# Kernel tuning notes

Measured on AMD Instinct MI355X. Metric: run time of the kernel, lower is better.

## Reference

```python
import jax, jax.numpy as jnp
import numpy as np

DEGREE_RES = 15
NUM_ROT = int(np.ceil(360 / DEGREE_RES))  # 24
PIXEL_SIZE = 0.0625
IM_METERS = 4.0
IM_SIZE = int(IM_METERS / PIXEL_SIZE)  # 64


def _create_rot_mat():
    angles = np.radians([i * DEGREE_RES for i in range(NUM_ROT)])
    c, s = np.cos(angles), np.sin(angles)
    rot = np.stack([
        np.stack([c, np.zeros_like(c), -s], axis=-1),
        np.stack([np.zeros_like(c), np.ones_like(c), np.zeros_like(c)], axis=-1),
        np.stack([s, np.zeros_like(c), c], axis=-1),
    ], axis=1)  # [NUM_ROT, 3, 3]
    return jnp.asarray(rot, dtype=jnp.float32)


def setup_inputs() -> dict:
    key = jax.random.key(0)
    xyz = jax.random.normal(key, (32, 16384, 3), dtype=jnp.float32)
    rot_mat = _create_rot_mat()
    return {"xyz": xyz, "rot_mat": rot_mat}


def reference(xyz, rot_mat):
    B, N, _ = xyz.shape
    R = rot_mat.shape[0]
    # rotate each point by each rotation: [B, R, N, 3]
    xyz_rot = jnp.einsum('rij,bnj->brni', rot_mat, xyz)
    # project x,z -> pixel indices (offset by half image extent, 2 meters)
    proj = jnp.round((xyz_rot[..., :2] + IM_METERS / 2) / PIXEL_SIZE).astype(jnp.int32)
    mask = ((proj[..., 0] >= 0) & (proj[..., 0] < IM_SIZE) &
            (proj[..., 1] >= 0) & (proj[..., 1] < IM_SIZE))
    # out-of-range points are zeroed -> they (faithfully) write at pixel (0,0)
    proj = proj * mask[..., None]
    vals = xyz_rot[..., 2] / 10.0  # non-occupancy branch: scatter z/10
    image = jnp.zeros((B, R, IM_SIZE, IM_SIZE), dtype=xyz.dtype)
    b = jnp.arange(B)[:, None, None]
    r = jnp.arange(R)[None, :, None]
    image = image.at[b, r, proj[..., 1], proj[..., 0]].set(vals)
    return image
```

## Files before the change

kernel.cpp:

```cpp
#include <hip/hip_runtime.h>
#include <stdint.h>

#define BB 32
#define NN 16384
#define RR 24
#define IMS 64
#define NPIX (IMS * IMS)
#define RPB 3
#define GROUPS (RR / RPB)
#define TOTAL_PIX (BB * RR * NPIX)

__global__ __launch_bounds__(1024) void rotproj_lds(
    const float* __restrict__ xyz, const float* __restrict__ rot,
    float* __restrict__ out) {
  __shared__ unsigned int img[RPB * NPIX];

  const int blk = blockIdx.x;
  const int b = blk >> 3;
  const int rg = blk & (GROUPS - 1);

  for (int i = threadIdx.x; i < RPB * NPIX; i += 1024) img[i] = 0u;

  const float* m = rot + rg * RPB * 9;
  float c0[RPB], c2[RPB], c6[RPB], c8[RPB];
#pragma unroll
  for (int rl = 0; rl < RPB; ++rl) {
    c0[rl] = m[rl * 9 + 0];
    c2[rl] = m[rl * 9 + 2];
    c6[rl] = m[rl * 9 + 6];
    c8[rl] = m[rl * 9 + 8];
  }

  __syncthreads();

  const float4* base4 = (const float4*)(xyz + (size_t)b * NN * 3);
  const int lane = threadIdx.x & 63;

#pragma unroll
  for (int iter = 0; iter < 2; ++iter) {
    const int n0 = iter * 8192 + threadIdx.x * 8;
    const int v = 6 * (n0 >> 3);
    const float4 f0 = base4[v + 0];
    const float4 f1 = base4[v + 1];
    const float4 f2 = base4[v + 2];
    const float4 f3 = base4[v + 3];
    const float4 f4 = base4[v + 4];
    const float4 f5 = base4[v + 5];

    const float xs[8] = {f0.x, f0.w, f1.z, f2.y, f3.x, f3.w, f4.z, f5.y};
    const float ys[8] = {f0.y, f1.x, f1.w, f2.z, f3.y, f4.x, f4.w, f5.z};
    const float zs[8] = {f0.z, f1.y, f2.x, f2.w, f3.z, f4.y, f5.x, f5.w};

    bool anyoob[RPB] = {false, false, false};
    unsigned int oobkey[RPB] = {0u, 0u, 0u};

#pragma unroll
    for (int j = 0; j < 8; ++j) {
      const float x = xs[j], y = ys[j], z = zs[j];

      const int py = (int)rintf(__fmaf_rn(y, 16.0f, 32.0f));
      const bool pyin = (unsigned)py < (unsigned)IMS;
      const unsigned int nkey = (unsigned)(n0 + j + 1) << 17;

#pragma unroll
      for (int rl = 0; rl < RPB; ++rl) {
        const float xr =
            __fadd_rn(__fmul_rn(c0[rl], x), __fmul_rn(c2[rl], z));
        const float zr =
            __fadd_rn(__fmul_rn(c6[rl], x), __fmul_rn(c8[rl], z));

        const int px = (int)rintf(__fmaf_rn(xr, 16.0f, 32.0f));
        const bool in = ((unsigned)px < (unsigned)IMS) & pyin;

        const unsigned int key = nkey | (__float_as_uint(zr) >> 15);

        if (in) {
          atomicMax(&img[rl * NPIX + py * IMS + px], key);
        } else {
          anyoob[rl] = true;
          oobkey[rl] = key;
        }
      }
    }

#pragma unroll
    for (int rl = 0; rl < RPB; ++rl) {
      const unsigned long long oob = __ballot(anyoob[rl]);
      if (anyoob[rl] && lane == 63 - __builtin_clzll(oob)) {
        atomicMax(&img[rl * NPIX], oobkey[rl]);
      }
    }
  }

  __syncthreads();

  float* oslice = out + ((size_t)b * RR + (size_t)rg * RPB) * NPIX;
#pragma unroll
  for (int t = 0; t < RPB * NPIX / 1024; ++t) {
    const int i = t * 1024 + threadIdx.x;
    const unsigned int k = img[i];
    const float zr = __uint_as_float((k & 0x1FFFFu) << 15);
    oslice[i] = k ? (zr / 10.0f) : 0.0f;
  }
}

extern "C" void kernel_launch(void* const* d_in, const int* in_sizes, int n_in,
                              void* d_out, int out_size, void* d_ws,
                              size_t ws_size, hipStream_t stream) {
  const float* xyz = (const float*)d_in[0];
  const float* rot = (const float*)d_in[1];
  float* out = (float*)d_out;

  rotproj_lds<<<BB * GROUPS, 1024, 0, stream>>>(xyz, rot, out);
}
```

Before: 70.36 us.

## Route out-of-bounds points to per-lane dump slots and process 16 contiguous points per thread

Out-of-range points now do an atomicMax into a per-lane dump slot in LDS instead of taking a divergent branch with per-iteration ballots. The dump slots are reduced with wave shuffles after the scatter pass and merged into pixel (0,0). Each thread now loads 12 contiguous float4s covering 16 points in one pass, replacing two iterations of 8 points. The final divide by 10 is replaced by a multiply by 0.1, which can differ from the reference in the last bit.

```diff
diff --git a/kernel.cpp b/kernel.cpp
--- a/kernel.cpp
+++ b/kernel.cpp
@@ -8,18 +8,19 @@
 #define NPIX (IMS * IMS)
 #define RPB 3
 #define GROUPS (RR / RPB)
-#define TOTAL_PIX (BB * RR * NPIX)
+#define DUMP_BASE (RPB * NPIX)
+#define LDS_WORDS (RPB * NPIX + RPB * 64)
 
 __global__ __launch_bounds__(1024) void rotproj_lds(
     const float* __restrict__ xyz, const float* __restrict__ rot,
     float* __restrict__ out) {
-  __shared__ unsigned int img[RPB * NPIX];
+  __shared__ unsigned int img[LDS_WORDS];
 
   const int blk = blockIdx.x;
   const int b = blk >> 3;
   const int rg = blk & (GROUPS - 1);
 
-  for (int i = threadIdx.x; i < RPB * NPIX; i += 1024) img[i] = 0u;
+  for (int i = threadIdx.x; i < LDS_WORDS; i += 1024) img[i] = 0u;
 
   const float* m = rot + rg * RPB * 9;
   float c0[RPB], c2[RPB], c6[RPB], c8[RPB];
@@ -34,73 +35,71 @@
   __syncthreads();
 
   const float4* base4 = (const float4*)(xyz + (size_t)b * NN * 3);
-  const int lane = threadIdx.x & 63;
+  const int t = threadIdx.x;
+  const int lane = t & 63;
+
+  float4 f[12];
+#pragma unroll
+  for (int i = 0; i < 12; ++i) f[i] = base4[12 * t + i];
+
+  float F[48];
+#pragma unroll
+  for (int i = 0; i < 12; ++i) {
+    F[4 * i + 0] = f[i].x;
+    F[4 * i + 1] = f[i].y;
+    F[4 * i + 2] = f[i].z;
+    F[4 * i + 3] = f[i].w;
+  }
 
 #pragma unroll
-  for (int iter = 0; iter < 2; ++iter) {
-    const int n0 = iter * 8192 + threadIdx.x * 8;
-    const int v = 6 * (n0 >> 3);
-    const float4 f0 = base4[v + 0];
-    const float4 f1 = base4[v + 1];
-    const float4 f2 = base4[v + 2];
-    const float4 f3 = base4[v + 3];
-    const float4 f4 = base4[v + 4];
-    const float4 f5 = base4[v + 5];
+  for (int k = 0; k < 16; ++k) {
+    const float x = F[3 * k + 0];
+    const float y = F[3 * k + 1];
+    const float z = F[3 * k + 2];
+    const int n = t * 16 + k;
 
-    const float xs[8] = {f0.x, f0.w, f1.z, f2.y, f3.x, f3.w, f4.z, f5.y};
-    const float ys[8] = {f0.y, f1.x, f1.w, f2.z, f3.y, f4.x, f4.w, f5.z};
-    const float zs[8] = {f0.z, f1.y, f2.x, f2.w, f3.z, f4.y, f5.x, f5.w};
-
-    bool anyoob[RPB] = {false, false, false};
-    unsigned int oobkey[RPB] = {0u, 0u, 0u};
-
-#pragma unroll
-    for (int j = 0; j < 8; ++j) {
-      const float x = xs[j], y = ys[j], z = zs[j];
-
-      const int py = (int)rintf(__fmaf_rn(y, 16.0f, 32.0f));
-      const bool pyin = (unsigned)py < (unsigned)IMS;
-      const unsigned int nkey = (unsigned)(n0 + j + 1) << 17;
-
-#pragma unroll
-      for (int rl = 0; rl < RPB; ++rl) {
-        const float xr =
-            __fadd_rn(__fmul_rn(c0[rl], x), __fmul_rn(c2[rl], z));
-        const float zr =
-            __fadd_rn(__fmul_rn(c6[rl], x), __fmul_rn(c8[rl], z));
-
-        const int px = (int)rintf(__fmaf_rn(xr, 16.0f, 32.0f));
-        const bool in = ((unsigned)px < (unsigned)IMS) & pyin;
-
-        const unsigned int key = nkey | (__float_as_uint(zr) >> 15);
-
-        if (in) {
-          atomicMax(&img[rl * NPIX + py * IMS + px], key);
-        } else {
-          anyoob[rl] = true;
-          oobkey[rl] = key;
-        }
-      }
-    }
+    const int py = (int)rintf(__fmaf_rn(y, 16.0f, 32.0f));
+    const bool pyin = (unsigned)py < (unsigned)IMS;
+    const unsigned int nkey = (unsigned)(n + 1) << 17;
 
 #pragma unroll
     for (int rl = 0; rl < RPB; ++rl) {
-      const unsigned long long oob = __ballot(anyoob[rl]);
-      if (anyoob[rl] && lane == 63 - __builtin_clzll(oob)) {
-        atomicMax(&img[rl * NPIX], oobkey[rl]);
-      }
+      const float xr = __fadd_rn(__fmul_rn(c0[rl], x), __fmul_rn(c2[rl], z));
+      const float zr = __fadd_rn(__fmul_rn(c6[rl], x), __fmul_rn(c8[rl], z));
+
+      const int px = (int)rintf(__fmaf_rn(xr, 16.0f, 32.0f));
+      const bool in = ((unsigned)px < (unsigned)IMS) & pyin;
+
+      const unsigned int key = nkey | (__float_as_uint(zr) >> 15);
+
+      const int addr =
+          in ? (rl * NPIX + py * IMS + px) : (DUMP_BASE + rl * 64 + lane);
+      atomicMax(&img[addr], key);
     }
+  }
+
+  __syncthreads();
+
+  const int wid = t >> 6;
+  if (wid < RPB) {
+    unsigned int v = img[DUMP_BASE + wid * 64 + lane];
+#pragma unroll
+    for (int o = 32; o >= 1; o >>= 1) {
+      const unsigned int u = (unsigned int)__shfl_xor((int)v, o, 64);
+      v = v > u ? v : u;
+    }
+    if (lane == 0) atomicMax(&img[wid * NPIX], v);
   }
 
   __syncthreads();
 
   float* oslice = out + ((size_t)b * RR + (size_t)rg * RPB) * NPIX;
 #pragma unroll
-  for (int t = 0; t < RPB * NPIX / 1024; ++t) {
-    const int i = t * 1024 + threadIdx.x;
+  for (int q = 0; q < RPB * NPIX / 1024; ++q) {
+    const int i = q * 1024 + t;
     const unsigned int k = img[i];
     const float zr = __uint_as_float((k & 0x1FFFFu) << 15);
-    oslice[i] = k ? (zr / 10.0f) : 0.0f;
+    oslice[i] = k ? (zr * 0.1f) : 0.0f;
   }
 }
 
```

After: 70.61 us. No clear change (+0.4%).
